# Performance work log

Measured on AMD Instinct MI355X. Metric: run time of the kernel, lower is better.

## Reference

```python
import jax, jax.numpy as jnp
import numpy as np

NUM_TASKS, IN_SIZE, OUT_SIZE, N_ROWS = 64, 512, 512, 2048


def setup_inputs() -> dict:
    key = jax.random.key(0)
    k_x, k_t, k_w = jax.random.split(key, 3)
    inputs = jax.random.normal(k_x, (N_ROWS, IN_SIZE), dtype=jnp.float32)
    task_ids = jax.random.randint(k_t, (N_ROWS,), 0, NUM_TASKS, dtype=jnp.int64)
    # in_size == out_size path: identity + N(0, 0.03) perturbation per task
    W = (jnp.eye(IN_SIZE, OUT_SIZE, dtype=jnp.float32)[None]
         + 0.03 * jax.random.normal(k_w, (NUM_TASKS, IN_SIZE, OUT_SIZE), dtype=jnp.float32))
    return {"inputs": inputs, "task_ids": task_ids, "W": W}


def reference(inputs, task_ids, W):
    # Gather the full per-row weight matrix then batched vector-matrix multiply,
    # faithful to torch.einsum('ni,nio->no', inputs, W[task_ids]).
    aligned = W[task_ids]                       # [I, in, out]
    return jnp.einsum("ni,nio->no", inputs, aligned)  # [I, out]
```

## Files before the change

### kernel.cpp

```cpp
#include <hip/hip_runtime.h>


#define NDIM 512
#define KDIM 512
#define MAXG 192

typedef _Float16 f16x8 __attribute__((ext_vector_type(8)));
typedef float    f32x4 __attribute__((ext_vector_type(4)));

__global__ __launch_bounds__(256) void k_groups(
    const int* __restrict__ tids, int n_rows,
    int* __restrict__ gtask, unsigned short* __restrict__ prow)
{
    __shared__ int cnt[64], pos[64], gbase[64];
    const int tid = threadIdx.x;
    if (tid < 64) { cnt[tid] = 0; pos[tid] = 0; }
    __syncthreads();
    for (int i = tid; i < n_rows; i += 256)
        atomicAdd(&cnt[tids[i]], 1);
    __syncthreads();
    if (tid == 0) {
        int off = 0;
        for (int t = 0; t < 64; ++t) {
            gbase[t] = off;
            off += (cnt[t] + 15) >> 4;
        }
    }
    __syncthreads();
    for (int i = tid; i < MAXG * 16; i += 256) prow[i] = 0xFFFFu;
    if (tid < MAXG) gtask[tid] = -1;
    __syncthreads();
    if (tid < 64) {
        const int ng = (cnt[tid] + 15) >> 4;
        for (int g = 0; g < ng; ++g) gtask[gbase[tid] + g] = tid;
    }
    for (int i = tid; i < n_rows; i += 256) {
        const int t = tids[i];
        const int p = atomicAdd(&pos[t], 1);
        prow[gbase[t] * 16 + p] = (unsigned short)i;
    }
}

__global__ __launch_bounds__(256, 4) void k_gemm(
    const float* __restrict__ x, const float* __restrict__ W,
    const int* __restrict__ gtask, const unsigned short* __restrict__ prow,
    float* __restrict__ out)
{
    const int tid  = threadIdx.x;
    const int lane = tid & 63;
    const int wv   = tid >> 6;
    const int ml   = lane & 15;
    const int q    = lane >> 4;
    const int c0   = blockIdx.x * 32;
    const int g    = blockIdx.y * 4 + wv;

    const int task = gtask[g];
    if (task < 0) return;

    const int rowreg = prow[g * 16 + ml];
    const int xrow   = (rowreg == 0xFFFF) ? 0 : rowreg;
    const float* xp = x + (size_t)xrow * KDIM + q * 8;
    const float* Wp = W + (size_t)task * KDIM * NDIM + (size_t)(q * 8) * NDIM + c0 + ml;

    f32x4 acc0 = {}, acc1 = {};
    #pragma unroll 2
    for (int kf = 0; kf < 16; ++kf) {
        const float* wk = Wp + (size_t)kf * 32 * NDIM;
        float b0[8], b1[8];
        #pragma unroll
        for (int j = 0; j < 8; ++j) {
            b0[j] = wk[(size_t)j * NDIM];
            b1[j] = wk[(size_t)j * NDIM + 16];
        }
        const float4 a0 = *(const float4*)(xp + kf * 32);
        const float4 a1 = *(const float4*)(xp + kf * 32 + 4);

        f16x8 af, bf0, bf1;
        af[0] = (_Float16)a0.x; af[1] = (_Float16)a0.y;
        af[2] = (_Float16)a0.z; af[3] = (_Float16)a0.w;
        af[4] = (_Float16)a1.x; af[5] = (_Float16)a1.y;
        af[6] = (_Float16)a1.z; af[7] = (_Float16)a1.w;
        #pragma unroll
        for (int j = 0; j < 8; ++j) {
            bf0[j] = (_Float16)b0[j];
            bf1[j] = (_Float16)b1[j];
        }
        acc0 = __builtin_amdgcn_mfma_f32_16x16x32_f16(af, bf0, acc0, 0, 0, 0);
        acc1 = __builtin_amdgcn_mfma_f32_16x16x32_f16(af, bf1, acc1, 0, 0, 0);
    }

    #pragma unroll
    for (int r2 = 0; r2 < 4; ++r2) {
        const int src  = q * 4 + r2;
        const int orow = __shfl(rowreg, src);
        if (orow != 0xFFFF) {
            out[(size_t)orow * NDIM + c0 + ml]      = acc0[r2];
            out[(size_t)orow * NDIM + c0 + 16 + ml] = acc1[r2];
        }
    }
}

extern "C" void kernel_launch(void* const* d_in, const int* in_sizes, int n_in,
                              void* d_out, int out_size, void* d_ws, size_t ws_size,
                              hipStream_t stream) {
    const float* x    = (const float*)d_in[0];
    const int*   tids = (const int*)d_in[1];
    const float* W    = (const float*)d_in[2];
    float*       out  = (float*)d_out;
    const int n_rows  = in_sizes[1];

    int*            gtask = (int*)d_ws;
    unsigned short* prow  = (unsigned short*)((char*)d_ws + 1024);

    k_groups<<<dim3(1), dim3(256), 0, stream>>>(tids, n_rows, gtask, prow);
    k_gemm<<<dim3(NDIM / 32, MAXG / 4), dim3(256), 0, stream>>>(x, W, gtask, prow, out);
}
```

Measured before the change: 119.1 us.

## Assign one block per task and stage task weights through LDS

Each block now handles a single task and a 32-column slice. It loads that task's W slice once, with coalesced float4 loads converted to fp16, into LDS in 128-k chunks using register prefetch. All row groups of the task reuse the staged chunk, where before each wave re-read W from global memory with strided scalar loads. The grouping kernel is simplified to per-task buckets of fixed capacity. In exchange, the grid is smaller (16x64 blocks), imbalanced tasks serialise their row groups inside one block, and each chunk adds syncthreads barriers.

```diff
diff --git a/kernel.cpp b/kernel.cpp
--- a/kernel.cpp
+++ b/kernel.cpp
@@ -3,47 +3,31 @@
 
 #define NDIM 512
 #define KDIM 512
-#define MAXG 192
 
 typedef _Float16 f16x8 __attribute__((ext_vector_type(8)));
+typedef _Float16 f16x4 __attribute__((ext_vector_type(4)));
 typedef float    f32x4 __attribute__((ext_vector_type(4)));
 
 __global__ __launch_bounds__(256) void k_groups(
     const int* __restrict__ tids, int n_rows,
-    int* __restrict__ gtask, unsigned short* __restrict__ prow)
+    int* __restrict__ gcnt, unsigned short* __restrict__ rows)
 {
-    __shared__ int cnt[64], pos[64], gbase[64];
+    __shared__ int cnt[64];
     const int tid = threadIdx.x;
-    if (tid < 64) { cnt[tid] = 0; pos[tid] = 0; }
+    if (tid < 64) cnt[tid] = 0;
     __syncthreads();
-    for (int i = tid; i < n_rows; i += 256)
-        atomicAdd(&cnt[tids[i]], 1);
-    __syncthreads();
-    if (tid == 0) {
-        int off = 0;
-        for (int t = 0; t < 64; ++t) {
-            gbase[t] = off;
-            off += (cnt[t] + 15) >> 4;
-        }
+    for (int i = tid; i < n_rows; i += 256) {
+        const int t = tids[i];
+        const int p = atomicAdd(&cnt[t], 1);
+        rows[t * 2048 + p] = (unsigned short)i;
     }
     __syncthreads();
-    for (int i = tid; i < MAXG * 16; i += 256) prow[i] = 0xFFFFu;
-    if (tid < MAXG) gtask[tid] = -1;
-    __syncthreads();
-    if (tid < 64) {
-        const int ng = (cnt[tid] + 15) >> 4;
-        for (int g = 0; g < ng; ++g) gtask[gbase[tid] + g] = tid;
-    }
-    for (int i = tid; i < n_rows; i += 256) {
-        const int t = tids[i];
-        const int p = atomicAdd(&pos[t], 1);
-        prow[gbase[t] * 16 + p] = (unsigned short)i;
-    }
+    if (tid < 64) gcnt[tid] = cnt[tid];
 }
 
 __global__ __launch_bounds__(256, 4) void k_gemm(
     const float* __restrict__ x, const float* __restrict__ W,
-    const int* __restrict__ gtask, const unsigned short* __restrict__ prow,
+    const int* __restrict__ gcnt, const unsigned short* __restrict__ rows,
     float* __restrict__ out)
 {
     const int tid  = threadIdx.x;
@@ -52,50 +36,92 @@
     const int ml   = lane & 15;
     const int q    = lane >> 4;
     const int c0   = blockIdx.x * 32;
-    const int g    = blockIdx.y * 4 + wv;
+    const int task = blockIdx.y;
 
-    const int task = gtask[g];
-    if (task < 0) return;
+    const int count = gcnt[task];
+    if (count == 0) return;
+    const int nh = (count + 63) >> 6;
 
-    const int rowreg = prow[g * 16 + ml];
-    const int xrow   = (rowreg == 0xFFFF) ? 0 : rowreg;
-    const float* xp = x + (size_t)xrow * KDIM + q * 8;
-    const float* Wp = W + (size_t)task * KDIM * NDIM + (size_t)(q * 8) * NDIM + c0 + ml;
+    __shared__ __align__(16) _Float16 Wt[16 * 33 * 8];
 
-    f32x4 acc0 = {}, acc1 = {};
-    #pragma unroll 2
-    for (int kf = 0; kf < 16; ++kf) {
-        const float* wk = Wp + (size_t)kf * 32 * NDIM;
-        float b0[8], b1[8];
+    const float*          Wg = W + (size_t)task * KDIM * NDIM + c0;
+    const unsigned short* rt = rows + task * 2048;
+
+    const int krun = tid >> 3;
+    const int sc4  = (tid & 7) * 4;
+
+    for (int h = 0; h < nh; ++h) {
+        const int j0 = h * 64 + wv * 16;
+        const int jj = j0 + ml;
+        const int rowreg = (jj < count) ? (int)rt[jj] : 0xFFFF;
+        const int xrow   = (rowreg == 0xFFFF) ? 0 : rowreg;
+        const float* xp  = x + (size_t)xrow * KDIM;
+        const bool wactive = (j0 < count);
+
+        f32x4 acc0 = {}, acc1 = {};
+
+        float4 wr[4];
         #pragma unroll
-        for (int j = 0; j < 8; ++j) {
-            b0[j] = wk[(size_t)j * NDIM];
-            b1[j] = wk[(size_t)j * NDIM + 16];
+        for (int j = 0; j < 4; ++j)
+            wr[j] = *(const float4*)(Wg + (size_t)(krun * 4 + j) * NDIM + sc4);
+
+        #pragma unroll
+        for (int gen = 0; gen < 4; ++gen) {
+            const int kb = gen * 128;
+
+            #pragma unroll
+            for (int j2 = 0; j2 < 4; ++j2) {
+                f16x4 v = {(_Float16)(((const float*)&wr[0])[j2]),
+                           (_Float16)(((const float*)&wr[1])[j2]),
+                           (_Float16)(((const float*)&wr[2])[j2]),
+                           (_Float16)(((const float*)&wr[3])[j2])};
+                const int c   = sc4 + j2;
+                const int idx = (((krun >> 1) * 33) + c) * 8 + (krun & 1) * 4;
+                *(f16x4*)&Wt[idx] = v;
+            }
+            __syncthreads();
+
+            float4 nwr[4];
+            if (gen < 3) {
+                #pragma unroll
+                for (int j = 0; j < 4; ++j)
+                    nwr[j] = *(const float4*)(Wg + (size_t)(kb + 128 + krun * 4 + j) * NDIM + sc4);
+            }
+
+            if (wactive) {
+                #pragma unroll
+                for (int ks = 0; ks < 4; ++ks) {
+                    const float4 a0 = *(const float4*)(xp + kb + ks * 32 + q * 8);
+                    const float4 a1 = *(const float4*)(xp + kb + ks * 32 + q * 8 + 4);
+                    f16x8 af;
+                    af[0] = (_Float16)a0.x; af[1] = (_Float16)a0.y;
+                    af[2] = (_Float16)a0.z; af[3] = (_Float16)a0.w;
+                    af[4] = (_Float16)a1.x; af[5] = (_Float16)a1.y;
+                    af[6] = (_Float16)a1.z; af[7] = (_Float16)a1.w;
+                    const int oct = ks * 4 + q;
+                    const f16x8 bf0 = *(const f16x8*)&Wt[(oct * 33 + ml) * 8];
+                    const f16x8 bf1 = *(const f16x8*)&Wt[(oct * 33 + 16 + ml) * 8];
+                    acc0 = __builtin_amdgcn_mfma_f32_16x16x32_f16(af, bf0, acc0, 0, 0, 0);
+                    acc1 = __builtin_amdgcn_mfma_f32_16x16x32_f16(af, bf1, acc1, 0, 0, 0);
+                }
+            }
+            __syncthreads();
+
+            if (gen < 3) {
+                #pragma unroll
+                for (int j = 0; j < 4; ++j) wr[j] = nwr[j];
+            }
         }
-        const float4 a0 = *(const float4*)(xp + kf * 32);
-        const float4 a1 = *(const float4*)(xp + kf * 32 + 4);
 
-        f16x8 af, bf0, bf1;
-        af[0] = (_Float16)a0.x; af[1] = (_Float16)a0.y;
-        af[2] = (_Float16)a0.z; af[3] = (_Float16)a0.w;
-        af[4] = (_Float16)a1.x; af[5] = (_Float16)a1.y;
-        af[6] = (_Float16)a1.z; af[7] = (_Float16)a1.w;
-        #pragma unroll
-        for (int j = 0; j < 8; ++j) {
-            bf0[j] = (_Float16)b0[j];
-            bf1[j] = (_Float16)b1[j];
-        }
-        acc0 = __builtin_amdgcn_mfma_f32_16x16x32_f16(af, bf0, acc0, 0, 0, 0);
-        acc1 = __builtin_amdgcn_mfma_f32_16x16x32_f16(af, bf1, acc1, 0, 0, 0);
-    }
-
-    #pragma unroll
-    for (int r2 = 0; r2 < 4; ++r2) {
-        const int src  = q * 4 + r2;
-        const int orow = __shfl(rowreg, src);
-        if (orow != 0xFFFF) {
-            out[(size_t)orow * NDIM + c0 + ml]      = acc0[r2];
-            out[(size_t)orow * NDIM + c0 + 16 + ml] = acc1[r2];
+        if (wactive) {
+            #pragma unroll
+            for (int rg = 0; rg < 4; ++rg) {
+                const int orow = __shfl(rowreg, q * 4 + rg);
+                if (orow != 0xFFFF) {
+                    out[(size_t)orow * NDIM + c0 + ml]      = acc0[rg];
+                    out[(size_t)orow * NDIM + c0 + 16 + ml] = acc1[rg];
+                }
+            }
         }
     }
 }
@@ -109,9 +135,9 @@
     float*       out  = (float*)d_out;
     const int n_rows  = in_sizes[1];
 
-    int*            gtask = (int*)d_ws;
-    unsigned short* prow  = (unsigned short*)((char*)d_ws + 1024);
+    int*            gcnt = (int*)d_ws;
+    unsigned short* rows = (unsigned short*)((char*)d_ws + 256);
 
-    k_groups<<<dim3(1), dim3(256), 0, stream>>>(tids, n_rows, gtask, prow);
-    k_gemm<<<dim3(NDIM / 32, MAXG / 4), dim3(256), 0, stream>>>(x, W, gtask, prow, out);
+    k_groups<<<dim3(1), dim3(256), 0, stream>>>(tids, n_rows, gcnt, rows);
+    k_gemm<<<dim3(NDIM / 32, 64), dim3(256), 0, stream>>>(x, W, gcnt, rows, out);
 }
```

After: 112.1 us. 5.9% less time.
